# Kernel tuning notes

Hardware: AMD Instinct MI355X
Metric: run time of the kernel (lower is better)

## Reference

```python
import jax, jax.numpy as jnp
import numpy as np

B, D, S, O = 32768, 1024, 64, 4  # batch, feature_dim, n_subjects, n_outputs


def setup_inputs() -> dict:
    key = jax.random.key(0)
    kx, ks, kw, kb = jax.random.split(key, 4)
    x = jax.random.normal(kx, (B, D), dtype=jnp.float32)          # backbone features
    subject_ids = jax.random.randint(ks, (B,), 0, S)              # per-sample head id
    W = jax.random.normal(kw, (S, D, O), dtype=jnp.float32) / np.float32(np.sqrt(D))
    b = jax.random.normal(kb, (S, O), dtype=jnp.float32) * 0.01
    return {"x": x, "subject_ids": subject_ids, "W": W, "b": b}


def reference(x, subject_ids, W, b):
    # Vectorized form of the per-subject loop:
    #   for sid in unique(subject_ids): outputs[idxs] = heads[sid](features[idxs])
    # Each head is Linear(D, O): out[i] = x[i] @ W[sid[i]] + b[sid[i]].
    Wg = jnp.take(W, subject_ids, axis=0)   # [B, D, O] gathered per-sample weights
    bg = jnp.take(b, subject_ids, axis=0)   # [B, O]
    return jnp.einsum('bd,bdo->bo', x, Wg) + bg
```

## Files before the change

### kernel.cpp

```cpp
#include <hip/hip_runtime.h>

constexpr int B = 32768;
constexpr int D = 1024;
constexpr int S = 64;
constexpr int O = 4;

constexpr int BLOCKS        = 2048;
constexpr int WAVES_TOTAL   = BLOCKS * 4;
constexpr int ROWS_PER_WAVE = B / WAVES_TOTAL;

__global__ __launch_bounds__(256) void main_kernel(
    const float* __restrict__ x,
    const int*   __restrict__ sid,
    const float* __restrict__ W,
    const float* __restrict__ bias,
    float*       __restrict__ out)
{
    const int lane = threadIdx.x & 63;
    const int wave = threadIdx.x >> 6;
    const int gw   = blockIdx.x * 4 + wave;
    const int q    = lane >> 4;

    int row = gw * ROWS_PER_WAVE;
    int s   = sid[row];

    const float*  xr = x + (size_t)row * D;
    const float4* Wr = (const float4*)(W + (size_t)s * (D * O));

    float  xb[2][4];
    float4 wb[2][4];

    #pragma unroll
    for (int j = 0; j < 4; ++j) xb[0][j] = xr[j * 64 + lane];
    #pragma unroll
    for (int j = 0; j < 4; ++j) wb[0][j] = Wr[j * 64 + lane];

    #pragma unroll 1
    for (int it = 0; it < ROWS_PER_WAVE; ++it) {
        const bool has_next = (it + 1 < ROWS_PER_WAVE);
        const int  s_next   = has_next ? sid[row + 1] : 0;

        float a0 = 0.f, a1 = 0.f, a2 = 0.f, a3 = 0.f;

        #pragma unroll
        for (int c = 0; c < 4; ++c) {
            const int cur = c & 1;
            const int nxt = cur ^ 1;

            if (c < 3) {
                const int base = (c + 1) * 256;
                #pragma unroll
                for (int j = 0; j < 4; ++j) xb[nxt][j] = xr[base + j * 64 + lane];
                #pragma unroll
                for (int j = 0; j < 4; ++j) wb[nxt][j] = Wr[base / 4 * 4 + j * 64 + lane];
            } else if (has_next) {
                const float*  xrn = x + (size_t)(row + 1) * D;
                const float4* Wrn = (const float4*)(W + (size_t)s_next * (D * O));
                #pragma unroll
                for (int j = 0; j < 4; ++j) xb[nxt][j] = xrn[j * 64 + lane];
                #pragma unroll
                for (int j = 0; j < 4; ++j) wb[nxt][j] = Wrn[j * 64 + lane];
            }

            #pragma unroll
            for (int j = 0; j < 4; ++j) {
                a0 += xb[cur][j] * wb[cur][j].x;
                a1 += xb[cur][j] * wb[cur][j].y;
                a2 += xb[cur][j] * wb[cur][j].z;
                a3 += xb[cur][j] * wb[cur][j].w;
            }
        }

        const float bb = bias[s * O + q];

        #pragma unroll
        for (int m = 16; m <= 32; m <<= 1) {
            a0 += __shfl_xor(a0, m, 64);
            a1 += __shfl_xor(a1, m, 64);
            a2 += __shfl_xor(a2, m, 64);
            a3 += __shfl_xor(a3, m, 64);
        }
        float v = (q == 0) ? a0 : (q == 1) ? a1 : (q == 2) ? a2 : a3;
        #pragma unroll
        for (int m = 1; m <= 8; m <<= 1)
            v += __shfl_xor(v, m, 64);

        if ((lane & 15) == 0)
            out[(size_t)row * O + q] = v + bb;

        row += 1;
        s    = s_next;
        xr   = x + (size_t)row * D;
        Wr   = (const float4*)(W + (size_t)s * (D * O));
    }
}

extern "C" void kernel_launch(void* const* d_in, const int* in_sizes, int n_in,
                              void* d_out, int out_size, void* d_ws, size_t ws_size,
                              hipStream_t stream) {
    const float* x    = (const float*)d_in[0];
    const int*   sid  = (const int*)d_in[1];
    const float* W    = (const float*)d_in[2];
    const float* bias = (const float*)d_in[3];
    float* out = (float*)d_out;

    main_kernel<<<BLOCKS, 256, 0, stream>>>(x, sid, W, bias, out);
}
```

Baseline: 204.1 us.

## Sort rows by subject and keep per-subject weights resident in registers

Adds a histogram/scan kernel and a scatter kernel that bucket row indices by subject id. The main kernel then walks rows in that sorted order and reloads the 16 KB weight slice into registers only when the subject changes, rather than streaming W alongside x for every row. The x reads become contiguous float4 loads per lane, and the grid is halved so each wave handles 8 rows. The cost is two extra small launches, global atomics in the scatter, and scattered row access into x.

```diff
diff --git a/kernel.cpp b/kernel.cpp
--- a/kernel.cpp
+++ b/kernel.cpp
@@ -5,94 +5,135 @@
 constexpr int S = 64;
 constexpr int O = 4;
 
-constexpr int BLOCKS        = 2048;
-constexpr int WAVES_TOTAL   = BLOCKS * 4;
-constexpr int ROWS_PER_WAVE = B / WAVES_TOTAL;
+
+constexpr int MAIN_BLOCKS   = 1024;
+constexpr int ROWS_PER_WAVE = B / (MAIN_BLOCKS * 4);
+
+__global__ __launch_bounds__(1024) void hist_scan_kernel(
+    const int* __restrict__ sid, int* __restrict__ cursors)
+{
+    __shared__ int h[S];
+    const int t = threadIdx.x;
+    if (t < S) h[t] = 0;
+    __syncthreads();
+    #pragma unroll 4
+    for (int i = t; i < B; i += 1024)
+        atomicAdd(&h[sid[i]], 1);
+    __syncthreads();
+    if (t < 64) {
+        const int v = h[t];
+        int xs = v;
+        #pragma unroll
+        for (int off = 1; off < 64; off <<= 1) {
+            const int y = __shfl_up(xs, off, 64);
+            if (t >= off) xs += y;
+        }
+        cursors[t] = xs - v;
+    }
+}
+
+__global__ __launch_bounds__(256) void scatter_kernel(
+    const int* __restrict__ sid, int* __restrict__ cursors,
+    unsigned* __restrict__ perm)
+{
+    for (int i = blockIdx.x * blockDim.x + threadIdx.x; i < B;
+         i += gridDim.x * blockDim.x) {
+        const int s = sid[i];
+        const int pos = atomicAdd(&cursors[s], 1);
+        perm[pos] = ((unsigned)s << 16) | (unsigned)i;
+    }
+}
 
 __global__ __launch_bounds__(256) void main_kernel(
-    const float* __restrict__ x,
-    const int*   __restrict__ sid,
-    const float* __restrict__ W,
-    const float* __restrict__ bias,
-    float*       __restrict__ out)
+    const float*    __restrict__ x,
+    const unsigned* __restrict__ perm,
+    const float*    __restrict__ W,
+    const float*    __restrict__ bias,
+    float*          __restrict__ out)
 {
     const int lane = threadIdx.x & 63;
     const int wave = threadIdx.x >> 6;
     const int gw   = blockIdx.x * 4 + wave;
     const int q    = lane >> 4;
 
-    int row = gw * ROWS_PER_WAVE;
-    int s   = sid[row];
+    int p = gw * ROWS_PER_WAVE;
+    const int pend = p + ROWS_PER_WAVE;
 
-    const float*  xr = x + (size_t)row * D;
-    const float4* Wr = (const float4*)(W + (size_t)s * (D * O));
+    const unsigned e = perm[p];
+    int s   = (int)__builtin_amdgcn_readfirstlane(e >> 16);
+    int row = (int)__builtin_amdgcn_readfirstlane(e & 0xFFFFu);
 
-    float  xb[2][4];
-    float4 wb[2][4];
+    float4 wreg[16];
+    {
+        const float4* Wp = (const float4*)(W + (size_t)s * (D * O));
+        #pragma unroll
+        for (int k = 0; k < 16; ++k) wreg[k] = Wp[lane * 16 + k];
+    }
 
-    #pragma unroll
-    for (int j = 0; j < 4; ++j) xb[0][j] = xr[j * 64 + lane];
-    #pragma unroll
-    for (int j = 0; j < 4; ++j) wb[0][j] = Wr[j * 64 + lane];
+    float4 xbA[4], xbB[4];
+    {
+        const float4* xr = (const float4*)(x + ((size_t)row << 10));
+        #pragma unroll
+        for (int j = 0; j < 4; ++j) xbA[j] = xr[(lane << 2) + j];
+    }
+
+#define PHASE(XC, XN)                                                          \
+    {                                                                          \
+        int s_next = s, row_next = row;                                        \
+        const bool more = (p + 1 < pend);                                      \
+        if (more) {                                                            \
+            const unsigned en = perm[p + 1];                                   \
+            s_next   = (int)__builtin_amdgcn_readfirstlane(en >> 16);          \
+            row_next = (int)__builtin_amdgcn_readfirstlane(en & 0xFFFFu);      \
+            const float4* xrn = (const float4*)(x + ((size_t)row_next << 10)); \
+            _Pragma("unroll")                                                  \
+            for (int j = 0; j < 4; ++j) XN[j] = xrn[(lane << 2) + j];          \
+        }                                                                      \
+        float a0 = 0.f, a1 = 0.f, a2 = 0.f, a3 = 0.f;                          \
+        _Pragma("unroll")                                                      \
+        for (int j = 0; j < 4; ++j) {                                          \
+            const float4 xv = XC[j];                                           \
+            const float4 w0 = wreg[4 * j + 0];                                 \
+            const float4 w1 = wreg[4 * j + 1];                                 \
+            const float4 w2 = wreg[4 * j + 2];                                 \
+            const float4 w3 = wreg[4 * j + 3];                                 \
+            a0 += xv.x * w0.x; a1 += xv.x * w0.y;                              \
+            a2 += xv.x * w0.z; a3 += xv.x * w0.w;                              \
+            a0 += xv.y * w1.x; a1 += xv.y * w1.y;                              \
+            a2 += xv.y * w1.z; a3 += xv.y * w1.w;                              \
+            a0 += xv.z * w2.x; a1 += xv.z * w2.y;                              \
+            a2 += xv.z * w2.z; a3 += xv.z * w2.w;                              \
+            a0 += xv.w * w3.x; a1 += xv.w * w3.y;                              \
+            a2 += xv.w * w3.z; a3 += xv.w * w3.w;                              \
+        }                                                                      \
+        const float bb = bias[(s << 2) + q];                                   \
+        _Pragma("unroll")                                                      \
+        for (int m = 16; m <= 32; m <<= 1) {                                   \
+            a0 += __shfl_xor(a0, m, 64);                                       \
+            a1 += __shfl_xor(a1, m, 64);                                       \
+            a2 += __shfl_xor(a2, m, 64);                                       \
+            a3 += __shfl_xor(a3, m, 64);                                       \
+        }                                                                      \
+        float v = (q == 0) ? a0 : (q == 1) ? a1 : (q == 2) ? a2 : a3;          \
+        _Pragma("unroll")                                                      \
+        for (int m = 1; m <= 8; m <<= 1)                                       \
+            v += __shfl_xor(v, m, 64);                                         \
+        if ((lane & 15) == 0)                                                  \
+            out[((size_t)row << 2) + q] = v + bb;                              \
+        if (more && s_next != s) {                                             \
+            const float4* Wp = (const float4*)(W + (size_t)s_next * (D * O));  \
+            _Pragma("unroll")                                                  \
+            for (int k = 0; k < 16; ++k) wreg[k] = Wp[lane * 16 + k];          \
+        }                                                                      \
+        s = s_next; row = row_next; ++p;                                       \
+    }
 
     #pragma unroll 1
-    for (int it = 0; it < ROWS_PER_WAVE; ++it) {
-        const bool has_next = (it + 1 < ROWS_PER_WAVE);
-        const int  s_next   = has_next ? sid[row + 1] : 0;
-
-        float a0 = 0.f, a1 = 0.f, a2 = 0.f, a3 = 0.f;
-
-        #pragma unroll
-        for (int c = 0; c < 4; ++c) {
-            const int cur = c & 1;
-            const int nxt = cur ^ 1;
-
-            if (c < 3) {
-                const int base = (c + 1) * 256;
-                #pragma unroll
-                for (int j = 0; j < 4; ++j) xb[nxt][j] = xr[base + j * 64 + lane];
-                #pragma unroll
-                for (int j = 0; j < 4; ++j) wb[nxt][j] = Wr[base / 4 * 4 + j * 64 + lane];
-            } else if (has_next) {
-                const float*  xrn = x + (size_t)(row + 1) * D;
-                const float4* Wrn = (const float4*)(W + (size_t)s_next * (D * O));
-                #pragma unroll
-                for (int j = 0; j < 4; ++j) xb[nxt][j] = xrn[j * 64 + lane];
-                #pragma unroll
-                for (int j = 0; j < 4; ++j) wb[nxt][j] = Wrn[j * 64 + lane];
-            }
-
-            #pragma unroll
-            for (int j = 0; j < 4; ++j) {
-                a0 += xb[cur][j] * wb[cur][j].x;
-                a1 += xb[cur][j] * wb[cur][j].y;
-                a2 += xb[cur][j] * wb[cur][j].z;
-                a3 += xb[cur][j] * wb[cur][j].w;
-            }
-        }
-
-        const float bb = bias[s * O + q];
-
-        #pragma unroll
-        for (int m = 16; m <= 32; m <<= 1) {
-            a0 += __shfl_xor(a0, m, 64);
-            a1 += __shfl_xor(a1, m, 64);
-            a2 += __shfl_xor(a2, m, 64);
-            a3 += __shfl_xor(a3, m, 64);
-        }
-        float v = (q == 0) ? a0 : (q == 1) ? a1 : (q == 2) ? a2 : a3;
-        #pragma unroll
-        for (int m = 1; m <= 8; m <<= 1)
-            v += __shfl_xor(v, m, 64);
-
-        if ((lane & 15) == 0)
-            out[(size_t)row * O + q] = v + bb;
-
-        row += 1;
-        s    = s_next;
-        xr   = x + (size_t)row * D;
-        Wr   = (const float4*)(W + (size_t)s * (D * O));
+    for (int it2 = 0; it2 < ROWS_PER_WAVE / 2; ++it2) {
+        PHASE(xbA, xbB)
+        PHASE(xbB, xbA)
     }
+#undef PHASE
 }
 
 extern "C" void kernel_launch(void* const* d_in, const int* in_sizes, int n_in,
@@ -104,5 +145,10 @@
     const float* bias = (const float*)d_in[3];
     float* out = (float*)d_out;
 
-    main_kernel<<<BLOCKS, 256, 0, stream>>>(x, sid, W, bias, out);
+    int*      cursors = (int*)d_ws;
+    unsigned* perm    = (unsigned*)(cursors + 64);
+
+    hist_scan_kernel<<<1, 1024, 0, stream>>>(sid, cursors);
+    scatter_kernel<<<128, 256, 0, stream>>>(sid, cursors, perm);
+    main_kernel<<<MAIN_BLOCKS, 256, 0, stream>>>(x, perm, W, bias, out);
 }
```

After: 267.8 us. 1.31x slower.

## Group rows by subject per block and stage subject weights in LDS

Applied to the files above, without the earlier changes.

Each block now owns one subject and one chunk of the batch. It stages that subject's weight matrix in shared memory, transposed so each output column is contiguous. Waves scan the subject ids with ballot/popcount to build a compacted list of matching rows, then compute dot products against the shared-memory weights while prefetching the next row. This replaces the per-row gather of 16 KB of weights from global or L2 with one load per block. The cost is that every block re-reads its whole chunk of subject ids (64x redundant id scans) and the load is uneven because rows per subject are random.

```diff
diff --git a/kernel.cpp b/kernel.cpp
--- a/kernel.cpp
+++ b/kernel.cpp
@@ -5,9 +5,11 @@
 constexpr int S = 64;
 constexpr int O = 4;
 
-constexpr int BLOCKS        = 2048;
-constexpr int WAVES_TOTAL   = BLOCKS * 4;
-constexpr int ROWS_PER_WAVE = B / WAVES_TOTAL;
+
+constexpr int CHUNKS      = 32;
+constexpr int CHUNK       = B / CHUNKS;
+constexpr int SEG         = CHUNK / 4;
+constexpr int MAIN_BLOCKS = S * CHUNKS;
 
 __global__ __launch_bounds__(256) void main_kernel(
     const float* __restrict__ x,
@@ -16,62 +18,84 @@
     const float* __restrict__ bias,
     float*       __restrict__ out)
 {
-    const int lane = threadIdx.x & 63;
-    const int wave = threadIdx.x >> 6;
-    const int gw   = blockIdx.x * 4 + wave;
+    __shared__ float Wt[O * D];
+    __shared__ int   list[4][SEG];
+
+    const int t    = threadIdx.x;
+    const int lane = t & 63;
+    const int wave = t >> 6;
+    const int s    = blockIdx.x >> 5;
+    const int c    = blockIdx.x & 31;
     const int q    = lane >> 4;
 
-    int row = gw * ROWS_PER_WAVE;
-    int s   = sid[row];
+    {
+        const float4* Wp = (const float4*)(W + (size_t)s * (D * O));
+        #pragma unroll
+        for (int r = 0; r < 4; ++r) {
+            const int d = r * 256 + t;
+            const float4 w4 = Wp[d];
+            Wt[0 * D + d] = w4.x;
+            Wt[1 * D + d] = w4.y;
+            Wt[2 * D + d] = w4.z;
+            Wt[3 * D + d] = w4.w;
+        }
+    }
 
-    const float*  xr = x + (size_t)row * D;
-    const float4* Wr = (const float4*)(W + (size_t)s * (D * O));
+    const int seg = c * CHUNK + wave * SEG;
+    int cnt = 0;
+    #pragma unroll
+    for (int r = 0; r < 4; ++r) {
+        const int i = seg + r * 64 + lane;
+        const bool m = (sid[i] == s);
+        const unsigned long long mask = __ballot(m);
+        const int rank = __popcll(mask & ((1ull << lane) - 1ull));
+        if (m) list[wave][cnt + rank] = i;
+        cnt += __popcll(mask);
+    }
 
-    float  xb[2][4];
-    float4 wb[2][4];
+    __syncthreads();
+    if (cnt == 0) return;
 
-    #pragma unroll
-    for (int j = 0; j < 4; ++j) xb[0][j] = xr[j * 64 + lane];
-    #pragma unroll
-    for (int j = 0; j < 4; ++j) wb[0][j] = Wr[j * 64 + lane];
+    const float   bb  = bias[(s << 2) + q];
+    const float4* Wt4 = (const float4*)Wt;
+
+    int rowC = __builtin_amdgcn_readfirstlane(list[wave][0]);
+    float4 xb[4];
+    {
+        const float4* xr = (const float4*)(x + ((size_t)rowC << 10));
+        #pragma unroll
+        for (int j = 0; j < 4; ++j) xb[j] = xr[64 * j + lane];
+    }
 
     #pragma unroll 1
-    for (int it = 0; it < ROWS_PER_WAVE; ++it) {
-        const bool has_next = (it + 1 < ROWS_PER_WAVE);
-        const int  s_next   = has_next ? sid[row + 1] : 0;
+    for (int k = 0; k < cnt; ++k) {
+        const bool more = (k + 1 < cnt);
+        const int rowN = more
+            ? __builtin_amdgcn_readfirstlane(list[wave][k + 1]) : rowC;
 
         float a0 = 0.f, a1 = 0.f, a2 = 0.f, a3 = 0.f;
-
         #pragma unroll
-        for (int c = 0; c < 4; ++c) {
-            const int cur = c & 1;
-            const int nxt = cur ^ 1;
-
-            if (c < 3) {
-                const int base = (c + 1) * 256;
-                #pragma unroll
-                for (int j = 0; j < 4; ++j) xb[nxt][j] = xr[base + j * 64 + lane];
-                #pragma unroll
-                for (int j = 0; j < 4; ++j) wb[nxt][j] = Wr[base / 4 * 4 + j * 64 + lane];
-            } else if (has_next) {
-                const float*  xrn = x + (size_t)(row + 1) * D;
-                const float4* Wrn = (const float4*)(W + (size_t)s_next * (D * O));
-                #pragma unroll
-                for (int j = 0; j < 4; ++j) xb[nxt][j] = xrn[j * 64 + lane];
-                #pragma unroll
-                for (int j = 0; j < 4; ++j) wb[nxt][j] = Wrn[j * 64 + lane];
-            }
-
-            #pragma unroll
-            for (int j = 0; j < 4; ++j) {
-                a0 += xb[cur][j] * wb[cur][j].x;
-                a1 += xb[cur][j] * wb[cur][j].y;
-                a2 += xb[cur][j] * wb[cur][j].z;
-                a3 += xb[cur][j] * wb[cur][j].w;
-            }
+        for (int j = 0; j < 4; ++j) {
+            const float4 xv = xb[j];
+            const float4 w0 = Wt4[0 * 256 + 64 * j + lane];
+            const float4 w1 = Wt4[1 * 256 + 64 * j + lane];
+            const float4 w2 = Wt4[2 * 256 + 64 * j + lane];
+            const float4 w3 = Wt4[3 * 256 + 64 * j + lane];
+            a0 += xv.x * w0.x; a1 += xv.x * w1.x;
+            a2 += xv.x * w2.x; a3 += xv.x * w3.x;
+            a0 += xv.y * w0.y; a1 += xv.y * w1.y;
+            a2 += xv.y * w2.y; a3 += xv.y * w3.y;
+            a0 += xv.z * w0.z; a1 += xv.z * w1.z;
+            a2 += xv.z * w2.z; a3 += xv.z * w3.z;
+            a0 += xv.w * w0.w; a1 += xv.w * w1.w;
+            a2 += xv.w * w2.w; a3 += xv.w * w3.w;
         }
 
-        const float bb = bias[s * O + q];
+        if (more) {
+            const float4* xr = (const float4*)(x + ((size_t)rowN << 10));
+            #pragma unroll
+            for (int j = 0; j < 4; ++j) xb[j] = xr[64 * j + lane];
+        }
 
         #pragma unroll
         for (int m = 16; m <= 32; m <<= 1) {
@@ -86,12 +110,9 @@
             v += __shfl_xor(v, m, 64);
 
         if ((lane & 15) == 0)
-            out[(size_t)row * O + q] = v + bb;
+            out[((size_t)rowC << 2) + q] = v + bb;
 
-        row += 1;
-        s    = s_next;
-        xr   = x + (size_t)row * D;
-        Wr   = (const float4*)(W + (size_t)s * (D * O));
+        rowC = rowN;
     }
 }
 
@@ -104,5 +125,5 @@
     const float* bias = (const float*)d_in[3];
     float* out = (float*)d_out;
 
-    main_kernel<<<BLOCKS, 256, 0, stream>>>(x, sid, W, bias, out);
+    main_kernel<<<MAIN_BLOCKS, 256, 0, stream>>>(x, sid, W, bias, out);
 }
```

After: 200.5 us. Within noise of the previous version (-1.8%).
